# Performance work log

Hardware: AMD Instinct MI355X
Metric: run time of the kernel (lower is better)

## Reference

```python
import jax, jax.numpy as jnp
import numpy as np

BN_EPS = 1e-5


def conv1x1(x, w, b):
    # x: [B,C,H,W], w: [O,C], b: [O]
    return jnp.einsum('oc,bchw->bohw', w, x) + b[None, :, None, None]


def setup_inputs() -> dict:
    key = jax.random.key(0)
    ks = jax.random.split(key, 8)
    B, C, H, W = 4, 256, 64, 64
    Ci = C // 2  # inter_channels
    std = 0.01
    return {
        'x': jax.random.normal(ks[0], (B, C, H, W), dtype=jnp.float32),
        'w_g': jax.random.normal(ks[1], (Ci, C), dtype=jnp.float32) * std,
        'b_g': jnp.zeros((Ci,), jnp.float32),
        'w_theta': jax.random.normal(ks[2], (Ci, C), dtype=jnp.float32) * std,
        'b_theta': jnp.zeros((Ci,), jnp.float32),
        'w_phi': jax.random.normal(ks[3], (Ci, C), dtype=jnp.float32) * std,
        'b_phi': jnp.zeros((Ci,), jnp.float32),
        'w_out': jax.random.normal(ks[4], (C, Ci), dtype=jnp.float32) * std,
        'b_out': jnp.zeros((C,), jnp.float32),
        'bn_gamma': jax.random.normal(ks[5], (C,), dtype=jnp.float32),
        'bn_beta': jnp.zeros((C,), jnp.float32),
    }


def reference(x, w_g, b_g, w_theta, b_theta, w_phi, b_phi, w_out, b_out, bn_gamma, bn_beta):
    B, C, H, W = x.shape
    Ci = w_g.shape[0]
    N = H * W
    # 1x1 conv projections -> flatten spatial to tokens
    g_x = conv1x1(x, w_g, b_g).reshape(B, Ci, N)          # [B,Ci,N]
    theta_x = conv1x1(x, w_theta, b_theta).reshape(B, Ci, N)
    phi_x = conv1x1(x, w_phi, b_phi).reshape(B, Ci, N)
    # dense non-causal attention over N=HW tokens (no scaling)
    f = jnp.einsum('bcn,bcm->bnm', theta_x, phi_x)        # [B,N,N]
    f_div_C = jax.nn.softmax(f, axis=-1)
    y = jnp.einsum('bnm,bcm->bcn', f_div_C, g_x)          # [B,Ci,N]
    y = y.reshape(B, Ci, H, W)
    # output 1x1 conv + BatchNorm2d (training mode: batch statistics)
    W_y = conv1x1(y, w_out, b_out)                        # [B,C,H,W]
    mean = W_y.mean(axis=(0, 2, 3))
    var = W_y.var(axis=(0, 2, 3))
    W_y = (W_y - mean[None, :, None, None]) * jax.lax.rsqrt(var + BN_EPS)[None, :, None, None]
    W_y = W_y * bn_gamma[None, :, None, None] + bn_beta[None, :, None, None]
    return W_y + x
```

## Files before the change

kernel.cpp:

```cpp
#include <hip/hip_runtime.h>

#define N_TOK 4096
#define C_IN 256
#define CI_ 128

typedef unsigned short u16;
typedef unsigned int   u32;
typedef __attribute__((ext_vector_type(8))) short bf16x8;
typedef __attribute__((ext_vector_type(4))) float f32x4;

__device__ __forceinline__ float lo16f(u32 u){ union{u32 i; float f;} c; c.i = u << 16; return c.f; }
__device__ __forceinline__ float hi16f(u32 u){ union{u32 i; float f;} c; c.i = u & 0xffff0000u; return c.f; }
__device__ __forceinline__ void bf8f(const uint4 u, float* f){
    f[0]=lo16f(u.x); f[1]=hi16f(u.x); f[2]=lo16f(u.y); f[3]=hi16f(u.y);
    f[4]=lo16f(u.z); f[5]=hi16f(u.z); f[6]=lo16f(u.w); f[7]=hi16f(u.w);
}
__device__ __forceinline__ float bf1f(u16 v){ union{u32 i; float f;} c; c.i = ((u32)v)<<16; return c.f; }
__device__ __forceinline__ u16 f2bf(float f){
    union{float f; u32 i;} c; c.f = f;
    u32 i = c.i;
    u32 r = (i + 0x7fffu + ((i >> 16) & 1u)) >> 16;
    return (u16)r;
}
__device__ __forceinline__ u32 packbf(float a, float b){
    return (u32)f2bf(a) | ((u32)f2bf(b) << 16);
}

__device__ __forceinline__ void load8(const void* base, size_t idx, int flag, float* f){
    if (flag) {
        const float* p = (const float*)base + idx;
        *(float4*)&f[0] = *(const float4*)p;
        *(float4*)&f[4] = *(const float4*)(p + 4);
    } else {
        uint4 u = *(const uint4*)((const u16*)base + idx);
        bf8f(u, f);
    }
}
__device__ __forceinline__ void load4(const void* base, size_t idx, int flag, float* f){
    if (flag) {
        float4 v = *(const float4*)((const float*)base + idx);
        f[0]=v.x; f[1]=v.y; f[2]=v.z; f[3]=v.w;
    } else {
        uint2 u = *(const uint2*)((const u16*)base + idx);
        f[0]=lo16f(u.x); f[1]=hi16f(u.x); f[2]=lo16f(u.y); f[3]=hi16f(u.y);
    }
}

__device__ __forceinline__ void dma16(const u16* g, char* l){
    __builtin_amdgcn_global_load_lds(
        (const __attribute__((address_space(1))) u32*)g,
        (__attribute__((address_space(3))) u32*)l, 16, 0, 0);
}

__global__ __launch_bounds__(256) void convert_params_kernel(
    const void* wg, const void* wt, const void* wp, const void* wo,
    const void* bg, const void* bt, const void* bp, const void* bo,
    const void* gm, const void* bt2,
    int* __restrict__ flagp, float* __restrict__ canon, u16* __restrict__ canon_bf,
    float* __restrict__ stats)
{
    __shared__ int sflag;
    const int tid = threadIdx.x;
    if (tid < 64) {
        int cnt = 0;
        const u16* wgp = (const u16*)wg;
        for (int i = tid; i < 256; i += 64) {
            u16 v = wgp[2 * i];
            if (((v >> 7) & 0xFF) >= 128) cnt++;
        }
        #pragma unroll
        for (int off = 32; off; off >>= 1) cnt += __shfl_down(cnt, off);
        if (tid == 0) sflag = (cnt >= 8) ? 1 : 0;
    }
    __syncthreads();
    const int f = sflag;
    if (blockIdx.x == 0 && tid == 0) *flagp = f;

    int idx = blockIdx.x * 256 + tid;
    if (idx >= 132224) {
        int j = idx - 132224;
        if (j < 4096) stats[j] = 0.f;
        return;
    }
    const void* src; int loc;
    if      (idx < 32768)  { src = wg;  loc = idx; }
    else if (idx < 65536)  { src = wt;  loc = idx - 32768; }
    else if (idx < 98304)  { src = wp;  loc = idx - 65536; }
    else if (idx < 131072) { src = wo;  loc = idx - 98304; }
    else if (idx < 131200) { src = bg;  loc = idx - 131072; }
    else if (idx < 131328) { src = bt;  loc = idx - 131200; }
    else if (idx < 131456) { src = bp;  loc = idx - 131328; }
    else if (idx < 131712) { src = bo;  loc = idx - 131456; }
    else if (idx < 131968) { src = gm;  loc = idx - 131712; }
    else                   { src = bt2; loc = idx - 131968; }
    float v = f ? ((const float*)src)[loc] : bf1f(((const u16*)src)[loc]);
    canon[idx] = v;
    if (idx < 131072) canon_bf[idx] = f2bf(v);
}

__global__ __launch_bounds__(256) void xpose_kernel(
    const void* __restrict__ x, const int* __restrict__ flagp, u16* __restrict__ xbfT)
{
    __shared__ u16 t[64][72];
    const int flag = *flagp;
    const int b = blockIdx.z, k0 = blockIdx.y * 64, n0 = blockIdx.x * 64;
    const int tid = threadIdx.x;
    const size_t xb = (size_t)b * C_IN * N_TOK;
    {
        int kk = tid >> 4, n4 = (tid & 15) * 4;
        #pragma unroll
        for (int i = 0; i < 4; ++i) {
            float f[4];
            load4(x, xb + (size_t)(k0 + kk + i * 16) * N_TOK + n0 + n4, flag, f);
            #pragma unroll
            for (int j = 0; j < 4; ++j) t[n4 + j][kk + i * 16] = f2bf(f[j]);
        }
    }
    __syncthreads();
    {
        int kq = tid & 3, n = tid >> 2;
        u16* dst = &xbfT[((size_t)b * N_TOK + n0 + n) * C_IN + k0 + kq * 16];
        *(uint4*)(dst + 0) = *(const uint4*)&t[n][kq * 16];
        *(uint4*)(dst + 8) = *(const uint4*)&t[n][kq * 16 + 8];
    }
}

__global__ __launch_bounds__(512) void proj_kernel(
    const u16* __restrict__ xbfT, const float* __restrict__ canon,
    const u16* __restrict__ wbf,
    u16* __restrict__ gbuf, u16* __restrict__ tbufT, u16* __restrict__ pbufT)
{
    __shared__ __align__(16) u16 plds[64 * 400];
    const int b  = blockIdx.y;
    const int n0 = blockIdx.x * 64;
    const int tid = threadIdx.x;
    const int w    = tid >> 6;
    const int lane = tid & 63;
    const int col  = lane & 15;
    const int quad = lane >> 4;
    const int rw   = w * 48;
    const size_t bN = (size_t)b * N_TOK;

    f32x4 acc[3][4];
    #pragma unroll
    for (int i = 0; i < 3; ++i)
        #pragma unroll
        for (int j = 0; j < 4; ++j) acc[i][j] = (f32x4){0.f,0.f,0.f,0.f};

    #pragma unroll
    for (int kc = 0; kc < 8; ++kc) {
        bf16x8 bfr[4];
        #pragma unroll
        for (int nf = 0; nf < 4; ++nf)
            bfr[nf] = *(const bf16x8*)&xbfT[(bN + n0 + nf * 16 + col) * C_IN + kc * 32 + quad * 8];
        #pragma unroll
        for (int rs = 0; rs < 3; ++rs) {
            bf16x8 afr = *(const bf16x8*)&wbf[(size_t)(rw + rs * 16 + col) * 256 + kc * 32 + quad * 8];
            #pragma unroll
            for (int nf = 0; nf < 4; ++nf)
                acc[rs][nf] = __builtin_amdgcn_mfma_f32_16x16x32_bf16(afr, bfr[nf], acc[rs][nf], 0, 0, 0);
        }
    }

    #pragma unroll
    for (int rs = 0; rs < 3; ++rs) {
        int r0 = rw + rs * 16 + quad * 4;
        float b0 = canon[131072 + r0 + 0];
        float b1 = canon[131072 + r0 + 1];
        float b2 = canon[131072 + r0 + 2];
        float b3 = canon[131072 + r0 + 3];
        #pragma unroll
        for (int nf = 0; nf < 4; ++nf) {
            int n = nf * 16 + col;
            uint2 pv;
            pv.x = packbf(acc[rs][nf][0] + b0, acc[rs][nf][1] + b1);
            pv.y = packbf(acc[rs][nf][2] + b2, acc[rs][nf][3] + b3);
            *(uint2*)&plds[n * 400 + r0] = pv;
        }
    }
    __syncthreads();

    {
        int r = tid & 127, nq = tid >> 7;
        u16 tmp[16];
        #pragma unroll
        for (int j = 0; j < 16; ++j) tmp[j] = plds[(nq * 16 + j) * 400 + r];
        u16* dst = &gbuf[((size_t)b * CI_ + r) * N_TOK + n0 + nq * 16];
        *(uint4*)(dst + 0) = *(uint4*)&tmp[0];
        *(uint4*)(dst + 8) = *(uint4*)&tmp[8];
    }
    {
        int n = tid & 63, part = tid >> 6;
        const u16* src = (part < 4) ? &plds[n * 400 + 128 + part * 32]
                                    : &plds[n * 400 + 256 + (part - 4) * 32];
        u16* dst = (part < 4) ? &tbufT[(bN + n0 + n) * CI_ + part * 32]
                              : &pbufT[(bN + n0 + n) * CI_ + (part - 4) * 32];
        #pragma unroll
        for (int v = 0; v < 4; ++v) *(uint4*)(dst + v * 8) = *(const uint4*)(src + v * 8);
    }
}

#define PB2   131072
#define MST2  147456
#define LST2  147712
#define SMEM2 147968

__global__ __launch_bounds__(512) void attn_kernel(
    const u16* __restrict__ tbufT, const u16* __restrict__ pbufT,
    const u16* __restrict__ gbuf,
    const u16* __restrict__ wbf, const float* __restrict__ canon,
    u16* __restrict__ wyb, float* __restrict__ stats)
{
    __shared__ __align__(16) char smem[SMEM2];
    const int b   = blockIdx.y;
    const int q0  = blockIdx.x * 64;
    const int tid = threadIdx.x;
    const int w    = tid >> 6;
    const int lane = tid & 63;
    const int col  = lane & 15;
    const int quad = lane >> 4;
    const int wq   = w & 3;
    const int ms   = w >> 2;
    const int qw   = wq * 16;
    const size_t bN = (size_t)b * N_TOK;
    const size_t bC = (size_t)b * CI_;

    bf16x8 thf[4];
    {
        const u16* tb = tbufT + (bN + q0 + qw + col) * CI_;
        #pragma unroll
        for (int kc = 0; kc < 4; ++kc)
            thf[kc] = *(const bf16x8*)(tb + kc * 32 + quad * 8);
    }

    const u16* sb[8];
    int ldso[8];
    int sstep;
    if (w < 4) {
        int r = lane >> 4, cp = lane & 15;
        sstep = 128 * CI_;
        #pragma unroll
        for (int j = 0; j < 8; ++j) {
            int seg = w * 8 + j, p = seg >> 4, m0 = (seg & 15) * 4;
            int m = m0 + r, h = cp ^ (m & 15);
            sb[j] = pbufT + (bN + p * 64 + m) * CI_ + h * 8;
            ldso[j] = p * 16384 + m0 * 256;
        }
    } else {
        int r = lane >> 3, cp = lane & 7;
        sstep = 128;
        #pragma unroll
        for (int j = 0; j < 8; ++j) {
            int seg = (w - 4) * 8 + j, p = seg >> 4, c0 = (seg & 15) * 8;
            int c = c0 + r, h = cp ^ (c & 7);
            sb[j] = gbuf + (bC + c) * N_TOK + p * 64 + h * 8;
            ldso[j] = 65536 + p * 16384 + c0 * 128;
        }
    }

    f32x4 yacc[8];
    #pragma unroll
    for (int i = 0; i < 8; ++i) yacc[i] = (f32x4){0.f, 0.f, 0.f, 0.f};
    float m_st = -3.0e38f, l_st = 0.f;

    #pragma unroll
    for (int j = 0; j < 8; ++j) dma16(sb[j], smem + ldso[j]);

    for (int s = 0; s < 32; ++s) {
        const int bb = (s & 1) << 15;
        __asm volatile("s_waitcnt lgkmcnt(0)" ::: "memory");
        __asm volatile("s_barrier" ::: "memory");
        if (s < 31) {
            const int nb = ((s + 1) & 1) << 15;
            const size_t so = (size_t)(s + 1) * sstep;
            #pragma unroll
            for (int j = 0; j < 8; ++j) dma16(sb[j] + so, smem + nb + ldso[j]);
            __asm volatile("s_waitcnt vmcnt(8)" ::: "memory");
        } else {
            __asm volatile("s_waitcnt vmcnt(0)" ::: "memory");
        }
        __asm volatile("s_barrier" ::: "memory");

        f32x4 sacc[4];
        #pragma unroll
        for (int i = 0; i < 4; ++i) sacc[i] = (f32x4){0.f, 0.f, 0.f, 0.f};
        #pragma unroll
        for (int kc = 0; kc < 4; ++kc) {
            #pragma unroll
            for (int msub = 0; msub < 4; ++msub) {
                int m = msub * 16 + col;
                int h = kc * 4 + quad;
                bf16x8 af = *(const bf16x8*)(smem + bb + ms * 16384 + m * 256 + ((h ^ (m & 15)) << 4));
                sacc[msub] = __builtin_amdgcn_mfma_f32_16x16x32_bf16(af, thf[kc], sacc[msub], 0, 0, 0);
            }
        }

        float tmax = sacc[0][0];
        #pragma unroll
        for (int i = 0; i < 4; ++i)
            #pragma unroll
            for (int r = 0; r < 4; ++r) tmax = fmaxf(tmax, sacc[i][r]);
        tmax = fmaxf(tmax, __shfl_xor(tmax, 16));
        tmax = fmaxf(tmax, __shfl_xor(tmax, 32));
        float m_new = fmaxf(m_st, tmax);
        float p16[16], ps = 0.f;
        #pragma unroll
        for (int i = 0; i < 4; ++i)
            #pragma unroll
            for (int r = 0; r < 4; ++r) {
                float pv = __expf(sacc[i][r] - m_new);
                p16[i * 4 + r] = pv;
                ps += pv;
            }
        ps += __shfl_xor(ps, 16);
        ps += __shfl_xor(ps, 32);
        float alpha = __expf(m_st - m_new);
        l_st = l_st * alpha + ps;
        m_st = m_new;
        #pragma unroll
        for (int i = 0; i < 8; ++i) {
            yacc[i][0] *= alpha; yacc[i][1] *= alpha;
            yacc[i][2] *= alpha; yacc[i][3] *= alpha;
        }

        {
            char* pb = smem + PB2 + w * 2048 + col * 128;
            #pragma unroll
            for (int msub = 0; msub < 4; ++msub) {
                #pragma unroll
                for (int pr = 0; pr < 2; ++pr) {
                    u32 d = packbf(p16[msub * 4 + pr * 2], p16[msub * 4 + pr * 2 + 1]);
                    int h = msub * 2 + (quad >> 1);
                    *(u32*)(pb + ((h ^ (col & 7)) << 4) + (quad & 1) * 8 + pr * 4) = d;
                }
            }
        }
        __asm volatile("s_waitcnt lgkmcnt(0)" ::: "memory");

        bf16x8 pf[2];
        #pragma unroll
        for (int km = 0; km < 2; ++km) {
            int h = km * 4 + quad;
            pf[km] = *(const bf16x8*)(smem + PB2 + w * 2048 + col * 128 + ((h ^ (col & 7)) << 4));
        }
        #pragma unroll
        for (int csub = 0; csub < 8; ++csub) {
            #pragma unroll
            for (int km = 0; km < 2; ++km) {
                int c = csub * 16 + col;
                int h = km * 4 + quad;
                bf16x8 gf = *(const bf16x8*)(smem + 65536 + bb + ms * 16384 + c * 128 + ((h ^ (c & 7)) << 4));
                yacc[csub] = __builtin_amdgcn_mfma_f32_16x16x32_bf16(gf, pf[km], yacc[csub], 0, 0, 0);
            }
        }
    }

    __syncthreads();
    if (ms == 1) {
        char* mb = smem + wq * 8192 + col * 512;
        #pragma unroll
        for (int csub = 0; csub < 8; ++csub)
            *(f32x4*)(mb + (((csub * 4 + quad) ^ col) << 4)) = yacc[csub];
        if (quad == 0) {
            *(float*)(smem + MST2 + (wq * 16 + col) * 4) = m_st;
            *(float*)(smem + LST2 + (wq * 16 + col) * 4) = l_st;
        }
    }
    __syncthreads();
    if (ms == 0) {
        float m1 = *(const float*)(smem + MST2 + (wq * 16 + col) * 4);
        float l1 = *(const float*)(smem + LST2 + (wq * 16 + col) * 4);
        float M  = fmaxf(m_st, m1);
        float a0 = __expf(m_st - M), a1 = __expf(m1 - M);
        float li = 1.f / (l_st * a0 + l1 * a1);
        float s0 = a0 * li, s1 = a1 * li;
        const char* mb = smem + wq * 8192 + col * 512;
        const int q = qw + col;
        #pragma unroll
        for (int csub = 0; csub < 8; ++csub) {
            f32x4 y1 = *(const f32x4*)(mb + (((csub * 4 + quad) ^ col) << 4));
            uint2 pv;
            pv.x = packbf(yacc[csub][0] * s0 + y1[0] * s1, yacc[csub][1] * s0 + y1[1] * s1);
            pv.y = packbf(yacc[csub][2] * s0 + y1[2] * s1, yacc[csub][3] * s0 + y1[3] * s1);
            int chunk = csub * 2 + (quad >> 1);
            *(uint2*)(smem + 32768 + q * 256 + ((chunk ^ (q & 15)) << 4) + (quad & 1) * 8) = pv;
        }
    }
    __syncthreads();

    const u16* wo = wbf + 98304;
    f32x4 oacc[2][4];
    #pragma unroll
    for (int i = 0; i < 2; ++i)
        #pragma unroll
        for (int j = 0; j < 4; ++j) oacc[i][j] = (f32x4){0.f,0.f,0.f,0.f};
    #pragma unroll
    for (int kc = 0; kc < 4; ++kc) {
        bf16x8 bqf[4];
        #pragma unroll
        for (int qf = 0; qf < 4; ++qf) {
            int q = qf * 16 + col;
            int h = kc * 4 + quad;
            bqf[qf] = *(const bf16x8*)(smem + 32768 + q * 256 + ((h ^ (q & 15)) << 4));
        }
        #pragma unroll
        for (int os = 0; os < 2; ++os) {
            bf16x8 afr = *(const bf16x8*)&wo[(size_t)(w * 32 + os * 16 + col) * CI_ + kc * 32 + quad * 8];
            #pragma unroll
            for (int qf = 0; qf < 4; ++qf)
                oacc[os][qf] = __builtin_amdgcn_mfma_f32_16x16x32_bf16(afr, bqf[qf], oacc[os][qf], 0, 0, 0);
        }
    }
    const int bucket = (blockIdx.x + blockIdx.y) & 7;
    float* sbk = stats + bucket * 512;
    #pragma unroll
    for (int os = 0; os < 2; ++os) {
        int ob = w * 32 + os * 16 + quad * 4;
        #pragma unroll
        for (int i = 0; i < 4; ++i) {
            float bb2 = canon[131456 + ob + i];
            float s1 = 0.f, s2 = 0.f;
            u16* dst = &wyb[((size_t)b * C_IN + ob + i) * N_TOK + q0 + col];
            #pragma unroll
            for (int qf = 0; qf < 4; ++qf) {
                float v = oacc[os][qf][i] + bb2;
                dst[qf * 16] = f2bf(v);
                s1 += v;
                s2 += v * v;
            }
            #pragma unroll
            for (int off = 8; off; off >>= 1) {
                s1 += __shfl_xor(s1, off);
                s2 += __shfl_xor(s2, off);
            }
            if (col == 0) {
                atomicAdd(&sbk[ob + i], s1);
                atomicAdd(&sbk[256 + ob + i], s2);
            }
        }
    }
}

__global__ __launch_bounds__(256) void bnorm_kernel(
    const u16* __restrict__ wyb, const void* __restrict__ x,
    const float* __restrict__ stats,
    const float* __restrict__ canon, const int* __restrict__ flagp,
    void* __restrict__ outv)
{
    const int flag = *flagp;
    size_t base = ((size_t)blockIdx.x * 256 + threadIdx.x) * 8;
    int o = (int)((base >> 12) & 255);
    float sum1 = 0.f, sum2 = 0.f;
    #pragma unroll
    for (int k = 0; k < 8; ++k) {
        sum1 += stats[k * 512 + o];
        sum2 += stats[k * 512 + 256 + o];
    }
    float mean = sum1 * (1.f / 16384.f);
    float var  = sum2 * (1.f / 16384.f) - mean * mean;
    float r = rsqrtf(var + 1e-5f);
    float gm = canon[131712 + o], bt = canon[131968 + o];
    uint4 wu = *(const uint4*)&wyb[base];
    float wv[8]; bf8f(wu, wv);
    float xf[8]; load8(x, base, flag, xf);
    float ov[8];
    #pragma unroll
    for (int i = 0; i < 8; ++i)
        ov[i] = (wv[i] - mean) * r * gm + bt + xf[i];
    if (flag) {
        float* op = (float*)outv + base;
        *(float4*)op       = *(float4*)&ov[0];
        *(float4*)(op + 4) = *(float4*)&ov[4];
    } else {
        uint4 res;
        res.x = packbf(ov[0], ov[1]);
        res.y = packbf(ov[2], ov[3]);
        res.z = packbf(ov[4], ov[5]);
        res.w = packbf(ov[6], ov[7]);
        *(uint4*)((u16*)outv + base) = res;
    }
}

extern "C" void kernel_launch(void* const* d_in, const int* in_sizes, int n_in,
                              void* d_out, int out_size, void* d_ws, size_t ws_size,
                              hipStream_t stream)
{
    const void* x   = d_in[0];
    const void* w_g = d_in[1];
    const void* b_g = d_in[2];
    const void* w_t = d_in[3];
    const void* b_t = d_in[4];
    const void* w_p = d_in[5];
    const void* b_p = d_in[6];
    const void* w_o = d_in[7];
    const void* b_o = d_in[8];
    const void* gm  = d_in[9];
    const void* bt  = d_in[10];

    char* base = (char*)d_ws;
    float* canon    = (float*)base;
    u16*   canon_bf = (u16*)(base + 528896);
    int*   flagp    = (int*)(base + 791040);
    float* stats    = (float*)(base + 791296);
    u16*   gbuf     = (u16*)(base + 1048576);
    u16*   tbufT    = (u16*)(base + 5242880);
    u16*   pbufT    = (u16*)(base + 9437184);
    u16*   wyb      = (u16*)(base + 13631488);
    u16*   xbfT     = (u16*)(base + 22020096);

    convert_params_kernel<<<533, 256, 0, stream>>>(w_g, w_t, w_p, w_o, b_g, b_t, b_p, b_o,
                                                   gm, bt, flagp, canon, canon_bf, stats);
    xpose_kernel<<<dim3(64, 4, 4), 256, 0, stream>>>(x, flagp, xbfT);
    proj_kernel<<<dim3(64, 4), 512, 0, stream>>>(xbfT, canon, canon_bf, gbuf, tbufT, pbufT);
    attn_kernel<<<dim3(64, 4), 512, 0, stream>>>(tbufT, pbufT, gbuf, canon_bf, canon, wyb, stats);
    bnorm_kernel<<<2048, 256, 0, stream>>>(wyb, x, stats, canon, flagp, d_out);
}
```

Before: 188.0 us.

## Fuse param conversion with transpose, and proj/attn/bnorm into one cooperative kernel

Merges the parameter-conversion and x-transpose kernels into a single prep launch, and fuses projection, attention and batch-norm into one cooperative kernel that uses grid-wide syncs in place of kernel boundaries. The aim is to remove launch overheads and inter-kernel gaps across the five-launch pipeline. In exchange it relies on all 256 blocks of 512 threads with about 148KB of shared memory each being co-resident. It also swaps kernel boundaries for grid barriers, and the bnorm phase now runs on only 256 blocks.

```diff
diff --git a/kernel.cpp b/kernel.cpp
--- a/kernel.cpp
+++ b/kernel.cpp
@@ -1,4 +1,6 @@
 #include <hip/hip_runtime.h>
+#include <hip/hip_cooperative_groups.h>
+namespace cg = cooperative_groups;
 
 #define N_TOK 4096
 #define C_IN 256
@@ -52,14 +54,15 @@
         (__attribute__((address_space(3))) u32*)l, 16, 0, 0);
 }
 
-__global__ __launch_bounds__(256) void convert_params_kernel(
-    const void* wg, const void* wt, const void* wp, const void* wo,
+__global__ __launch_bounds__(256) void prep_kernel(
+    const void* x, const void* wg, const void* wt, const void* wp, const void* wo,
     const void* bg, const void* bt, const void* bp, const void* bo,
     const void* gm, const void* bt2,
     int* __restrict__ flagp, float* __restrict__ canon, u16* __restrict__ canon_bf,
-    float* __restrict__ stats)
+    float* __restrict__ stats, u16* __restrict__ xbfT)
 {
     __shared__ int sflag;
+    __shared__ u16 t[64][72];
     const int tid = threadIdx.x;
     if (tid < 64) {
         int cnt = 0;
@@ -73,411 +76,404 @@
         if (tid == 0) sflag = (cnt >= 8) ? 1 : 0;
     }
     __syncthreads();
-    const int f = sflag;
-    if (blockIdx.x == 0 && tid == 0) *flagp = f;
-
-    int idx = blockIdx.x * 256 + tid;
-    if (idx >= 132224) {
-        int j = idx - 132224;
-        if (j < 4096) stats[j] = 0.f;
-        return;
-    }
-    const void* src; int loc;
-    if      (idx < 32768)  { src = wg;  loc = idx; }
-    else if (idx < 65536)  { src = wt;  loc = idx - 32768; }
-    else if (idx < 98304)  { src = wp;  loc = idx - 65536; }
-    else if (idx < 131072) { src = wo;  loc = idx - 98304; }
-    else if (idx < 131200) { src = bg;  loc = idx - 131072; }
-    else if (idx < 131328) { src = bt;  loc = idx - 131200; }
-    else if (idx < 131456) { src = bp;  loc = idx - 131328; }
-    else if (idx < 131712) { src = bo;  loc = idx - 131456; }
-    else if (idx < 131968) { src = gm;  loc = idx - 131712; }
-    else                   { src = bt2; loc = idx - 131968; }
-    float v = f ? ((const float*)src)[loc] : bf1f(((const u16*)src)[loc]);
-    canon[idx] = v;
-    if (idx < 131072) canon_bf[idx] = f2bf(v);
-}
-
-__global__ __launch_bounds__(256) void xpose_kernel(
-    const void* __restrict__ x, const int* __restrict__ flagp, u16* __restrict__ xbfT)
-{
-    __shared__ u16 t[64][72];
-    const int flag = *flagp;
-    const int b = blockIdx.z, k0 = blockIdx.y * 64, n0 = blockIdx.x * 64;
-    const int tid = threadIdx.x;
-    const size_t xb = (size_t)b * C_IN * N_TOK;
-    {
-        int kk = tid >> 4, n4 = (tid & 15) * 4;
-        #pragma unroll
-        for (int i = 0; i < 4; ++i) {
-            float f[4];
-            load4(x, xb + (size_t)(k0 + kk + i * 16) * N_TOK + n0 + n4, flag, f);
-            #pragma unroll
-            for (int j = 0; j < 4; ++j) t[n4 + j][kk + i * 16] = f2bf(f[j]);
-        }
-    }
-    __syncthreads();
-    {
-        int kq = tid & 3, n = tid >> 2;
-        u16* dst = &xbfT[((size_t)b * N_TOK + n0 + n) * C_IN + k0 + kq * 16];
-        *(uint4*)(dst + 0) = *(const uint4*)&t[n][kq * 16];
-        *(uint4*)(dst + 8) = *(const uint4*)&t[n][kq * 16 + 8];
-    }
-}
-
-__global__ __launch_bounds__(512) void proj_kernel(
+    const int flag = sflag;
+    const int bid = blockIdx.x;
+
+    if (bid < 549) {
+        if (bid == 0 && tid == 0) *flagp = flag;
+        int idx = bid * 256 + tid;
+        if (idx >= 132224) {
+            int j = idx - 132224;
+            if (j < 4096) stats[j] = 0.f;
+            return;
+        }
+        const void* src; int loc;
+        if      (idx < 32768)  { src = wg;  loc = idx; }
+        else if (idx < 65536)  { src = wt;  loc = idx - 32768; }
+        else if (idx < 98304)  { src = wp;  loc = idx - 65536; }
+        else if (idx < 131072) { src = wo;  loc = idx - 98304; }
+        else if (idx < 131200) { src = bg;  loc = idx - 131072; }
+        else if (idx < 131328) { src = bt;  loc = idx - 131200; }
+        else if (idx < 131456) { src = bp;  loc = idx - 131328; }
+        else if (idx < 131712) { src = bo;  loc = idx - 131456; }
+        else if (idx < 131968) { src = gm;  loc = idx - 131712; }
+        else                   { src = bt2; loc = idx - 131968; }
+        float v = flag ? ((const float*)src)[loc] : bf1f(((const u16*)src)[loc]);
+        canon[idx] = v;
+        if (idx < 131072) canon_bf[idx] = f2bf(v);
+    } else {
+        int tb = bid - 549;
+        int nb = tb & 63, kb = (tb >> 6) & 3, b = tb >> 8;
+        const int k0 = kb * 64, n0 = nb * 64;
+        const size_t xb = (size_t)b * C_IN * N_TOK;
+        {
+            int kk = tid >> 4, n4 = (tid & 15) * 4;
+            #pragma unroll
+            for (int i = 0; i < 4; ++i) {
+                float f[4];
+                load4(x, xb + (size_t)(k0 + kk + i * 16) * N_TOK + n0 + n4, flag, f);
+                #pragma unroll
+                for (int j = 0; j < 4; ++j) t[n4 + j][kk + i * 16] = f2bf(f[j]);
+            }
+        }
+        __syncthreads();
+        {
+            int kq = tid & 3, n = tid >> 2;
+            u16* dst = &xbfT[((size_t)b * N_TOK + n0 + n) * C_IN + k0 + kq * 16];
+            *(uint4*)(dst + 0) = *(const uint4*)&t[n][kq * 16];
+            *(uint4*)(dst + 8) = *(const uint4*)&t[n][kq * 16 + 8];
+        }
+    }
+}
+
+#define PB2   131072
+#define MST2  147456
+#define LST2  147712
+#define SMEM2 147968
+
+__global__ __launch_bounds__(512) void mega_kernel(
     const u16* __restrict__ xbfT, const float* __restrict__ canon,
     const u16* __restrict__ wbf,
-    u16* __restrict__ gbuf, u16* __restrict__ tbufT, u16* __restrict__ pbufT)
+    u16* __restrict__ gbuf, u16* __restrict__ tbufT, u16* __restrict__ pbufT,
+    u16* __restrict__ wyb, float* __restrict__ stats,
+    const void* __restrict__ x, const int* __restrict__ flagp,
+    void* __restrict__ outv)
 {
-    __shared__ __align__(16) u16 plds[64 * 400];
-    const int b  = blockIdx.y;
-    const int n0 = blockIdx.x * 64;
+    __shared__ __align__(16) char smem[SMEM2];
+    cg::grid_group grid = cg::this_grid();
+    const int bx  = blockIdx.x;
+    const int b   = blockIdx.y;
     const int tid = threadIdx.x;
     const int w    = tid >> 6;
     const int lane = tid & 63;
     const int col  = lane & 15;
     const int quad = lane >> 4;
-    const int rw   = w * 48;
-    const size_t bN = (size_t)b * N_TOK;
-
-    f32x4 acc[3][4];
-    #pragma unroll
-    for (int i = 0; i < 3; ++i)
-        #pragma unroll
-        for (int j = 0; j < 4; ++j) acc[i][j] = (f32x4){0.f,0.f,0.f,0.f};
-
-    #pragma unroll
-    for (int kc = 0; kc < 8; ++kc) {
-        bf16x8 bfr[4];
-        #pragma unroll
-        for (int nf = 0; nf < 4; ++nf)
-            bfr[nf] = *(const bf16x8*)&xbfT[(bN + n0 + nf * 16 + col) * C_IN + kc * 32 + quad * 8];
-        #pragma unroll
-        for (int rs = 0; rs < 3; ++rs) {
-            bf16x8 afr = *(const bf16x8*)&wbf[(size_t)(rw + rs * 16 + col) * 256 + kc * 32 + quad * 8];
-            #pragma unroll
-            for (int nf = 0; nf < 4; ++nf)
-                acc[rs][nf] = __builtin_amdgcn_mfma_f32_16x16x32_bf16(afr, bfr[nf], acc[rs][nf], 0, 0, 0);
-        }
-    }
-
-    #pragma unroll
-    for (int rs = 0; rs < 3; ++rs) {
-        int r0 = rw + rs * 16 + quad * 4;
-        float b0 = canon[131072 + r0 + 0];
-        float b1 = canon[131072 + r0 + 1];
-        float b2 = canon[131072 + r0 + 2];
-        float b3 = canon[131072 + r0 + 3];
-        #pragma unroll
-        for (int nf = 0; nf < 4; ++nf) {
-            int n = nf * 16 + col;
-            uint2 pv;
-            pv.x = packbf(acc[rs][nf][0] + b0, acc[rs][nf][1] + b1);
-            pv.y = packbf(acc[rs][nf][2] + b2, acc[rs][nf][3] + b3);
-            *(uint2*)&plds[n * 400 + r0] = pv;
-        }
-    }
-    __syncthreads();
-
-    {
-        int r = tid & 127, nq = tid >> 7;
-        u16 tmp[16];
-        #pragma unroll
-        for (int j = 0; j < 16; ++j) tmp[j] = plds[(nq * 16 + j) * 400 + r];
-        u16* dst = &gbuf[((size_t)b * CI_ + r) * N_TOK + n0 + nq * 16];
-        *(uint4*)(dst + 0) = *(uint4*)&tmp[0];
-        *(uint4*)(dst + 8) = *(uint4*)&tmp[8];
-    }
-    {
-        int n = tid & 63, part = tid >> 6;
-        const u16* src = (part < 4) ? &plds[n * 400 + 128 + part * 32]
-                                    : &plds[n * 400 + 256 + (part - 4) * 32];
-        u16* dst = (part < 4) ? &tbufT[(bN + n0 + n) * CI_ + part * 32]
-                              : &pbufT[(bN + n0 + n) * CI_ + (part - 4) * 32];
-        #pragma unroll
-        for (int v = 0; v < 4; ++v) *(uint4*)(dst + v * 8) = *(const uint4*)(src + v * 8);
-    }
-}
-
-#define PB2   131072
-#define MST2  147456
-#define LST2  147712
-#define SMEM2 147968
-
-__global__ __launch_bounds__(512) void attn_kernel(
-    const u16* __restrict__ tbufT, const u16* __restrict__ pbufT,
-    const u16* __restrict__ gbuf,
-    const u16* __restrict__ wbf, const float* __restrict__ canon,
-    u16* __restrict__ wyb, float* __restrict__ stats)
-{
-    __shared__ __align__(16) char smem[SMEM2];
-    const int b   = blockIdx.y;
-    const int q0  = blockIdx.x * 64;
-    const int tid = threadIdx.x;
-    const int w    = tid >> 6;
-    const int lane = tid & 63;
-    const int col  = lane & 15;
-    const int quad = lane >> 4;
-    const int wq   = w & 3;
-    const int ms   = w >> 2;
-    const int qw   = wq * 16;
     const size_t bN = (size_t)b * N_TOK;
     const size_t bC = (size_t)b * CI_;
 
-    bf16x8 thf[4];
     {
-        const u16* tb = tbufT + (bN + q0 + qw + col) * CI_;
-        #pragma unroll
-        for (int kc = 0; kc < 4; ++kc)
-            thf[kc] = *(const bf16x8*)(tb + kc * 32 + quad * 8);
-    }
-
-    const u16* sb[8];
-    int ldso[8];
-    int sstep;
-    if (w < 4) {
-        int r = lane >> 4, cp = lane & 15;
-        sstep = 128 * CI_;
-        #pragma unroll
-        for (int j = 0; j < 8; ++j) {
-            int seg = w * 8 + j, p = seg >> 4, m0 = (seg & 15) * 4;
-            int m = m0 + r, h = cp ^ (m & 15);
-            sb[j] = pbufT + (bN + p * 64 + m) * CI_ + h * 8;
-            ldso[j] = p * 16384 + m0 * 256;
-        }
-    } else {
-        int r = lane >> 3, cp = lane & 7;
-        sstep = 128;
-        #pragma unroll
-        for (int j = 0; j < 8; ++j) {
-            int seg = (w - 4) * 8 + j, p = seg >> 4, c0 = (seg & 15) * 8;
-            int c = c0 + r, h = cp ^ (c & 7);
-            sb[j] = gbuf + (bC + c) * N_TOK + p * 64 + h * 8;
-            ldso[j] = 65536 + p * 16384 + c0 * 128;
-        }
-    }
-
-    f32x4 yacc[8];
-    #pragma unroll
-    for (int i = 0; i < 8; ++i) yacc[i] = (f32x4){0.f, 0.f, 0.f, 0.f};
-    float m_st = -3.0e38f, l_st = 0.f;
-
-    #pragma unroll
-    for (int j = 0; j < 8; ++j) dma16(sb[j], smem + ldso[j]);
-
-    for (int s = 0; s < 32; ++s) {
-        const int bb = (s & 1) << 15;
-        __asm volatile("s_waitcnt lgkmcnt(0)" ::: "memory");
-        __asm volatile("s_barrier" ::: "memory");
-        if (s < 31) {
-            const int nb = ((s + 1) & 1) << 15;
-            const size_t so = (size_t)(s + 1) * sstep;
-            #pragma unroll
-            for (int j = 0; j < 8; ++j) dma16(sb[j] + so, smem + nb + ldso[j]);
-            __asm volatile("s_waitcnt vmcnt(8)" ::: "memory");
+        u16* plds = (u16*)smem;
+        const int n0 = bx * 64;
+        const int rw = w * 48;
+        f32x4 acc[3][4];
+        #pragma unroll
+        for (int i = 0; i < 3; ++i)
+            #pragma unroll
+            for (int j = 0; j < 4; ++j) acc[i][j] = (f32x4){0.f,0.f,0.f,0.f};
+
+        #pragma unroll
+        for (int kc = 0; kc < 8; ++kc) {
+            bf16x8 bfr[4];
+            #pragma unroll
+            for (int nf = 0; nf < 4; ++nf)
+                bfr[nf] = *(const bf16x8*)&xbfT[(bN + n0 + nf * 16 + col) * C_IN + kc * 32 + quad * 8];
+            #pragma unroll
+            for (int rs = 0; rs < 3; ++rs) {
+                bf16x8 afr = *(const bf16x8*)&wbf[(size_t)(rw + rs * 16 + col) * 256 + kc * 32 + quad * 8];
+                #pragma unroll
+                for (int nf = 0; nf < 4; ++nf)
+                    acc[rs][nf] = __builtin_amdgcn_mfma_f32_16x16x32_bf16(afr, bfr[nf], acc[rs][nf], 0, 0, 0);
+            }
+        }
+        #pragma unroll
+        for (int rs = 0; rs < 3; ++rs) {
+            int r0 = rw + rs * 16 + quad * 4;
+            float b0 = canon[131072 + r0 + 0];
+            float b1 = canon[131072 + r0 + 1];
+            float b2 = canon[131072 + r0 + 2];
+            float b3 = canon[131072 + r0 + 3];
+            #pragma unroll
+            for (int nf = 0; nf < 4; ++nf) {
+                int n = nf * 16 + col;
+                uint2 pv;
+                pv.x = packbf(acc[rs][nf][0] + b0, acc[rs][nf][1] + b1);
+                pv.y = packbf(acc[rs][nf][2] + b2, acc[rs][nf][3] + b3);
+                *(uint2*)&plds[n * 400 + r0] = pv;
+            }
+        }
+        __syncthreads();
+        {
+            int r = tid & 127, nq = tid >> 7;
+            u16 tmp[16];
+            #pragma unroll
+            for (int j = 0; j < 16; ++j) tmp[j] = plds[(nq * 16 + j) * 400 + r];
+            u16* dst = &gbuf[(bC + r) * N_TOK + n0 + nq * 16];
+            *(uint4*)(dst + 0) = *(uint4*)&tmp[0];
+            *(uint4*)(dst + 8) = *(uint4*)&tmp[8];
+        }
+        {
+            int n = tid & 63, part = tid >> 6;
+            const u16* src = (part < 4) ? &plds[n * 400 + 128 + part * 32]
+                                        : &plds[n * 400 + 256 + (part - 4) * 32];
+            u16* dst = (part < 4) ? &tbufT[(bN + n0 + n) * CI_ + part * 32]
+                                  : &pbufT[(bN + n0 + n) * CI_ + (part - 4) * 32];
+            #pragma unroll
+            for (int v = 0; v < 4; ++v) *(uint4*)(dst + v * 8) = *(const uint4*)(src + v * 8);
+        }
+    }
+    grid.sync();
+
+    {
+        const int q0 = bx * 64;
+        const int wq = w & 3;
+        const int ms = w >> 2;
+        const int qw = wq * 16;
+
+        bf16x8 thf[4];
+        {
+            const u16* tb = tbufT + (bN + q0 + qw + col) * CI_;
+            #pragma unroll
+            for (int kc = 0; kc < 4; ++kc)
+                thf[kc] = *(const bf16x8*)(tb + kc * 32 + quad * 8);
+        }
+
+        const u16* sbp[8];
+        int ldso[8];
+        int sstep;
+        if (w < 4) {
+            int r = lane >> 4, cp = lane & 15;
+            sstep = 128 * CI_;
+            #pragma unroll
+            for (int j = 0; j < 8; ++j) {
+                int seg = w * 8 + j, p = seg >> 4, m0 = (seg & 15) * 4;
+                int m = m0 + r, h = cp ^ (m & 15);
+                sbp[j] = pbufT + (bN + p * 64 + m) * CI_ + h * 8;
+                ldso[j] = p * 16384 + m0 * 256;
+            }
         } else {
-            __asm volatile("s_waitcnt vmcnt(0)" ::: "memory");
-        }
-        __asm volatile("s_barrier" ::: "memory");
-
-        f32x4 sacc[4];
-        #pragma unroll
-        for (int i = 0; i < 4; ++i) sacc[i] = (f32x4){0.f, 0.f, 0.f, 0.f};
+            int r = lane >> 3, cp = lane & 7;
+            sstep = 128;
+            #pragma unroll
+            for (int j = 0; j < 8; ++j) {
+                int seg = (w - 4) * 8 + j, p = seg >> 4, c0 = (seg & 15) * 8;
+                int c = c0 + r, h = cp ^ (c & 7);
+                sbp[j] = gbuf + (bC + c) * N_TOK + p * 64 + h * 8;
+                ldso[j] = 65536 + p * 16384 + c0 * 128;
+            }
+        }
+
+        f32x4 yacc[8];
+        #pragma unroll
+        for (int i = 0; i < 8; ++i) yacc[i] = (f32x4){0.f, 0.f, 0.f, 0.f};
+        float m_st = -3.0e38f, l_st = 0.f;
+
+        #pragma unroll
+        for (int j = 0; j < 8; ++j) dma16(sbp[j], smem + ldso[j]);
+
+        for (int s = 0; s < 32; ++s) {
+            const int bb = (s & 1) << 15;
+            __asm volatile("s_waitcnt lgkmcnt(0)" ::: "memory");
+            __asm volatile("s_barrier" ::: "memory");
+            if (s < 31) {
+                const int nb = ((s + 1) & 1) << 15;
+                const size_t so = (size_t)(s + 1) * sstep;
+                #pragma unroll
+                for (int j = 0; j < 8; ++j) dma16(sbp[j] + so, smem + nb + ldso[j]);
+                __asm volatile("s_waitcnt vmcnt(8)" ::: "memory");
+            } else {
+                __asm volatile("s_waitcnt vmcnt(0)" ::: "memory");
+            }
+            __asm volatile("s_barrier" ::: "memory");
+
+            f32x4 sacc[4];
+            #pragma unroll
+            for (int i = 0; i < 4; ++i) sacc[i] = (f32x4){0.f, 0.f, 0.f, 0.f};
+            #pragma unroll
+            for (int kc = 0; kc < 4; ++kc) {
+                #pragma unroll
+                for (int msub = 0; msub < 4; ++msub) {
+                    int m = msub * 16 + col;
+                    int h = kc * 4 + quad;
+                    bf16x8 af = *(const bf16x8*)(smem + bb + ms * 16384 + m * 256 + ((h ^ (m & 15)) << 4));
+                    sacc[msub] = __builtin_amdgcn_mfma_f32_16x16x32_bf16(af, thf[kc], sacc[msub], 0, 0, 0);
+                }
+            }
+
+            float tmax = sacc[0][0];
+            #pragma unroll
+            for (int i = 0; i < 4; ++i)
+                #pragma unroll
+                for (int r = 0; r < 4; ++r) tmax = fmaxf(tmax, sacc[i][r]);
+            tmax = fmaxf(tmax, __shfl_xor(tmax, 16));
+            tmax = fmaxf(tmax, __shfl_xor(tmax, 32));
+            float m_new = fmaxf(m_st, tmax);
+            float p16[16], ps = 0.f;
+            #pragma unroll
+            for (int i = 0; i < 4; ++i)
+                #pragma unroll
+                for (int r = 0; r < 4; ++r) {
+                    float pv = __expf(sacc[i][r] - m_new);
+                    p16[i * 4 + r] = pv;
+                    ps += pv;
+                }
+            ps += __shfl_xor(ps, 16);
+            ps += __shfl_xor(ps, 32);
+            float alpha = __expf(m_st - m_new);
+            l_st = l_st * alpha + ps;
+            m_st = m_new;
+            #pragma unroll
+            for (int i = 0; i < 8; ++i) {
+                yacc[i][0] *= alpha; yacc[i][1] *= alpha;
+                yacc[i][2] *= alpha; yacc[i][3] *= alpha;
+            }
+
+            {
+                char* pb = smem + PB2 + w * 2048 + col * 128;
+                #pragma unroll
+                for (int msub = 0; msub < 4; ++msub) {
+                    #pragma unroll
+                    for (int pr = 0; pr < 2; ++pr) {
+                        u32 d = packbf(p16[msub * 4 + pr * 2], p16[msub * 4 + pr * 2 + 1]);
+                        int h = msub * 2 + (quad >> 1);
+                        *(u32*)(pb + ((h ^ (col & 7)) << 4) + (quad & 1) * 8 + pr * 4) = d;
+                    }
+                }
+            }
+            __asm volatile("s_waitcnt lgkmcnt(0)" ::: "memory");
+
+            bf16x8 pf[2];
+            #pragma unroll
+            for (int km = 0; km < 2; ++km) {
+                int h = km * 4 + quad;
+                pf[km] = *(const bf16x8*)(smem + PB2 + w * 2048 + col * 128 + ((h ^ (col & 7)) << 4));
+            }
+            #pragma unroll
+            for (int csub = 0; csub < 8; ++csub) {
+                #pragma unroll
+                for (int km = 0; km < 2; ++km) {
+                    int c = csub * 16 + col;
+                    int h = km * 4 + quad;
+                    bf16x8 gf = *(const bf16x8*)(smem + 65536 + bb + ms * 16384 + c * 128 + ((h ^ (c & 7)) << 4));
+                    yacc[csub] = __builtin_amdgcn_mfma_f32_16x16x32_bf16(gf, pf[km], yacc[csub], 0, 0, 0);
+                }
+            }
+        }
+
+        __syncthreads();
+        if (ms == 1) {
+            char* mb = smem + wq * 8192 + col * 512;
+            #pragma unroll
+            for (int csub = 0; csub < 8; ++csub)
+                *(f32x4*)(mb + (((csub * 4 + quad) ^ col) << 4)) = yacc[csub];
+            if (quad == 0) {
+                *(float*)(smem + MST2 + (wq * 16 + col) * 4) = m_st;
+                *(float*)(smem + LST2 + (wq * 16 + col) * 4) = l_st;
+            }
+        }
+        __syncthreads();
+        if (ms == 0) {
+            float m1 = *(const float*)(smem + MST2 + (wq * 16 + col) * 4);
+            float l1 = *(const float*)(smem + LST2 + (wq * 16 + col) * 4);
+            float M  = fmaxf(m_st, m1);
+            float a0 = __expf(m_st - M), a1 = __expf(m1 - M);
+            float li = 1.f / (l_st * a0 + l1 * a1);
+            float s0 = a0 * li, s1 = a1 * li;
+            const char* mb = smem + wq * 8192 + col * 512;
+            const int q = qw + col;
+            #pragma unroll
+            for (int csub = 0; csub < 8; ++csub) {
+                f32x4 y1 = *(const f32x4*)(mb + (((csub * 4 + quad) ^ col) << 4));
+                uint2 pv;
+                pv.x = packbf(yacc[csub][0] * s0 + y1[0] * s1, yacc[csub][1] * s0 + y1[1] * s1);
+                pv.y = packbf(yacc[csub][2] * s0 + y1[2] * s1, yacc[csub][3] * s0 + y1[3] * s1);
+                int chunk = csub * 2 + (quad >> 1);
+                *(uint2*)(smem + 32768 + q * 256 + ((chunk ^ (q & 15)) << 4) + (quad & 1) * 8) = pv;
+            }
+        }
+        __syncthreads();
+
+        const u16* wo = wbf + 98304;
+        f32x4 oacc[2][4];
+        #pragma unroll
+        for (int i = 0; i < 2; ++i)
+            #pragma unroll
+            for (int j = 0; j < 4; ++j) oacc[i][j] = (f32x4){0.f,0.f,0.f,0.f};
         #pragma unroll
         for (int kc = 0; kc < 4; ++kc) {
-            #pragma unroll
-            for (int msub = 0; msub < 4; ++msub) {
-                int m = msub * 16 + col;
+            bf16x8 bqf[4];
+            #pragma unroll
+            for (int qf = 0; qf < 4; ++qf) {
+                int q = qf * 16 + col;
                 int h = kc * 4 + quad;
-                bf16x8 af = *(const bf16x8*)(smem + bb + ms * 16384 + m * 256 + ((h ^ (m & 15)) << 4));
-                sacc[msub] = __builtin_amdgcn_mfma_f32_16x16x32_bf16(af, thf[kc], sacc[msub], 0, 0, 0);
-            }
-        }
-
-        float tmax = sacc[0][0];
-        #pragma unroll
-        for (int i = 0; i < 4; ++i)
-            #pragma unroll
-            for (int r = 0; r < 4; ++r) tmax = fmaxf(tmax, sacc[i][r]);
-        tmax = fmaxf(tmax, __shfl_xor(tmax, 16));
-        tmax = fmaxf(tmax, __shfl_xor(tmax, 32));
-        float m_new = fmaxf(m_st, tmax);
-        float p16[16], ps = 0.f;
-        #pragma unroll
-        for (int i = 0; i < 4; ++i)
-            #pragma unroll
-            for (int r = 0; r < 4; ++r) {
-                float pv = __expf(sacc[i][r] - m_new);
-                p16[i * 4 + r] = pv;
-                ps += pv;
-            }
-        ps += __shfl_xor(ps, 16);
-        ps += __shfl_xor(ps, 32);
-        float alpha = __expf(m_st - m_new);
-        l_st = l_st * alpha + ps;
-        m_st = m_new;
-        #pragma unroll
-        for (int i = 0; i < 8; ++i) {
-            yacc[i][0] *= alpha; yacc[i][1] *= alpha;
-            yacc[i][2] *= alpha; yacc[i][3] *= alpha;
-        }
-
-        {
-            char* pb = smem + PB2 + w * 2048 + col * 128;
-            #pragma unroll
-            for (int msub = 0; msub < 4; ++msub) {
-                #pragma unroll
-                for (int pr = 0; pr < 2; ++pr) {
-                    u32 d = packbf(p16[msub * 4 + pr * 2], p16[msub * 4 + pr * 2 + 1]);
-                    int h = msub * 2 + (quad >> 1);
-                    *(u32*)(pb + ((h ^ (col & 7)) << 4) + (quad & 1) * 8 + pr * 4) = d;
-                }
-            }
-        }
-        __asm volatile("s_waitcnt lgkmcnt(0)" ::: "memory");
-
-        bf16x8 pf[2];
-        #pragma unroll
-        for (int km = 0; km < 2; ++km) {
-            int h = km * 4 + quad;
-            pf[km] = *(const bf16x8*)(smem + PB2 + w * 2048 + col * 128 + ((h ^ (col & 7)) << 4));
-        }
-        #pragma unroll
-        for (int csub = 0; csub < 8; ++csub) {
-            #pragma unroll
-            for (int km = 0; km < 2; ++km) {
-                int c = csub * 16 + col;
-                int h = km * 4 + quad;
-                bf16x8 gf = *(const bf16x8*)(smem + 65536 + bb + ms * 16384 + c * 128 + ((h ^ (c & 7)) << 4));
-                yacc[csub] = __builtin_amdgcn_mfma_f32_16x16x32_bf16(gf, pf[km], yacc[csub], 0, 0, 0);
-            }
-        }
-    }
-
-    __syncthreads();
-    if (ms == 1) {
-        char* mb = smem + wq * 8192 + col * 512;
-        #pragma unroll
-        for (int csub = 0; csub < 8; ++csub)
-            *(f32x4*)(mb + (((csub * 4 + quad) ^ col) << 4)) = yacc[csub];
-        if (quad == 0) {
-            *(float*)(smem + MST2 + (wq * 16 + col) * 4) = m_st;
-            *(float*)(smem + LST2 + (wq * 16 + col) * 4) = l_st;
-        }
-    }
-    __syncthreads();
-    if (ms == 0) {
-        float m1 = *(const float*)(smem + MST2 + (wq * 16 + col) * 4);
-        float l1 = *(const float*)(smem + LST2 + (wq * 16 + col) * 4);
-        float M  = fmaxf(m_st, m1);
-        float a0 = __expf(m_st - M), a1 = __expf(m1 - M);
-        float li = 1.f / (l_st * a0 + l1 * a1);
-        float s0 = a0 * li, s1 = a1 * li;
-        const char* mb = smem + wq * 8192 + col * 512;
-        const int q = qw + col;
-        #pragma unroll
-        for (int csub = 0; csub < 8; ++csub) {
-            f32x4 y1 = *(const f32x4*)(mb + (((csub * 4 + quad) ^ col) << 4));
-            uint2 pv;
-            pv.x = packbf(yacc[csub][0] * s0 + y1[0] * s1, yacc[csub][1] * s0 + y1[1] * s1);
-            pv.y = packbf(yacc[csub][2] * s0 + y1[2] * s1, yacc[csub][3] * s0 + y1[3] * s1);
-            int chunk = csub * 2 + (quad >> 1);
-            *(uint2*)(smem + 32768 + q * 256 + ((chunk ^ (q & 15)) << 4) + (quad & 1) * 8) = pv;
-        }
-    }
-    __syncthreads();
-
-    const u16* wo = wbf + 98304;
-    f32x4 oacc[2][4];
-    #pragma unroll
-    for (int i = 0; i < 2; ++i)
-        #pragma unroll
-        for (int j = 0; j < 4; ++j) oacc[i][j] = (f32x4){0.f,0.f,0.f,0.f};
-    #pragma unroll
-    for (int kc = 0; kc < 4; ++kc) {
-        bf16x8 bqf[4];
-        #pragma unroll
-        for (int qf = 0; qf < 4; ++qf) {
-            int q = qf * 16 + col;
-            int h = kc * 4 + quad;
-            bqf[qf] = *(const bf16x8*)(smem + 32768 + q * 256 + ((h ^ (q & 15)) << 4));
-        }
+                bqf[qf] = *(const bf16x8*)(smem + 32768 + q * 256 + ((h ^ (q & 15)) << 4));
+            }
+            #pragma unroll
+            for (int os = 0; os < 2; ++os) {
+                bf16x8 afr = *(const bf16x8*)&wo[(size_t)(w * 32 + os * 16 + col) * CI_ + kc * 32 + quad * 8];
+                #pragma unroll
+                for (int qf = 0; qf < 4; ++qf)
+                    oacc[os][qf] = __builtin_amdgcn_mfma_f32_16x16x32_bf16(afr, bqf[qf], oacc[os][qf], 0, 0, 0);
+            }
+        }
+        const int bucket = (bx + b) & 7;
+        float* sbk = stats + bucket * 512;
         #pragma unroll
         for (int os = 0; os < 2; ++os) {
-            bf16x8 afr = *(const bf16x8*)&wo[(size_t)(w * 32 + os * 16 + col) * CI_ + kc * 32 + quad * 8];
-            #pragma unroll
-            for (int qf = 0; qf < 4; ++qf)
-                oacc[os][qf] = __builtin_amdgcn_mfma_f32_16x16x32_bf16(afr, bqf[qf], oacc[os][qf], 0, 0, 0);
-        }
-    }
-    const int bucket = (blockIdx.x + blockIdx.y) & 7;
-    float* sbk = stats + bucket * 512;
-    #pragma unroll
-    for (int os = 0; os < 2; ++os) {
-        int ob = w * 32 + os * 16 + quad * 4;
-        #pragma unroll
-        for (int i = 0; i < 4; ++i) {
-            float bb2 = canon[131456 + ob + i];
-            float s1 = 0.f, s2 = 0.f;
-            u16* dst = &wyb[((size_t)b * C_IN + ob + i) * N_TOK + q0 + col];
-            #pragma unroll
-            for (int qf = 0; qf < 4; ++qf) {
-                float v = oacc[os][qf][i] + bb2;
-                dst[qf * 16] = f2bf(v);
-                s1 += v;
-                s2 += v * v;
-            }
-            #pragma unroll
-            for (int off = 8; off; off >>= 1) {
-                s1 += __shfl_xor(s1, off);
-                s2 += __shfl_xor(s2, off);
-            }
-            if (col == 0) {
-                atomicAdd(&sbk[ob + i], s1);
-                atomicAdd(&sbk[256 + ob + i], s2);
-            }
-        }
-    }
-}
-
-__global__ __launch_bounds__(256) void bnorm_kernel(
-    const u16* __restrict__ wyb, const void* __restrict__ x,
-    const float* __restrict__ stats,
-    const float* __restrict__ canon, const int* __restrict__ flagp,
-    void* __restrict__ outv)
-{
-    const int flag = *flagp;
-    size_t base = ((size_t)blockIdx.x * 256 + threadIdx.x) * 8;
-    int o = (int)((base >> 12) & 255);
-    float sum1 = 0.f, sum2 = 0.f;
-    #pragma unroll
-    for (int k = 0; k < 8; ++k) {
-        sum1 += stats[k * 512 + o];
-        sum2 += stats[k * 512 + 256 + o];
-    }
-    float mean = sum1 * (1.f / 16384.f);
-    float var  = sum2 * (1.f / 16384.f) - mean * mean;
-    float r = rsqrtf(var + 1e-5f);
-    float gm = canon[131712 + o], bt = canon[131968 + o];
-    uint4 wu = *(const uint4*)&wyb[base];
-    float wv[8]; bf8f(wu, wv);
-    float xf[8]; load8(x, base, flag, xf);
-    float ov[8];
-    #pragma unroll
-    for (int i = 0; i < 8; ++i)
-        ov[i] = (wv[i] - mean) * r * gm + bt + xf[i];
-    if (flag) {
-        float* op = (float*)outv + base;
-        *(float4*)op       = *(float4*)&ov[0];
-        *(float4*)(op + 4) = *(float4*)&ov[4];
-    } else {
-        uint4 res;
-        res.x = packbf(ov[0], ov[1]);
-        res.y = packbf(ov[2], ov[3]);
-        res.z = packbf(ov[4], ov[5]);
-        res.w = packbf(ov[6], ov[7]);
-        *(uint4*)((u16*)outv + base) = res;
+            int ob = w * 32 + os * 16 + quad * 4;
+            #pragma unroll
+            for (int i = 0; i < 4; ++i) {
+                float bb2 = canon[131456 + ob + i];
+                float s1 = 0.f, s2 = 0.f;
+                u16* dst = &wyb[((size_t)b * C_IN + ob + i) * N_TOK + q0 + col];
+                #pragma unroll
+                for (int qf = 0; qf < 4; ++qf) {
+                    float v = oacc[os][qf][i] + bb2;
+                    dst[qf * 16] = f2bf(v);
+                    s1 += v;
+                    s2 += v * v;
+                }
+                #pragma unroll
+                for (int off = 8; off; off >>= 1) {
+                    s1 += __shfl_xor(s1, off);
+                    s2 += __shfl_xor(s2, off);
+                }
+                if (col == 0) {
+                    atomicAdd(&sbk[ob + i], s1);
+                    atomicAdd(&sbk[256 + ob + i], s2);
+                }
+            }
+        }
+    }
+    grid.sync();
+
+    {
+        const int flag = *flagp;
+        const int o = bx * 4 + (tid >> 7);
+        const int l128 = tid & 127;
+        float sum1 = 0.f, sum2 = 0.f;
+        #pragma unroll
+        for (int k = 0; k < 8; ++k) {
+            sum1 += stats[k * 512 + o];
+            sum2 += stats[k * 512 + 256 + o];
+        }
+        float mean = sum1 * (1.f / 16384.f);
+        float var  = sum2 * (1.f / 16384.f) - mean * mean;
+        float r = rsqrtf(var + 1e-5f);
+        float gmv = canon[131712 + o], btv = canon[131968 + o];
+        const size_t rowb = ((size_t)b * C_IN + o) * N_TOK;
+        #pragma unroll
+        for (int j = 0; j < 4; ++j) {
+            size_t base = rowb + (size_t)l128 * 32 + j * 8;
+            uint4 wu = *(const uint4*)&wyb[base];
+            float wv[8]; bf8f(wu, wv);
+            float xf[8]; load8(x, base, flag, xf);
+            float ov[8];
+            #pragma unroll
+            for (int i = 0; i < 8; ++i)
+                ov[i] = (wv[i] - mean) * r * gmv + btv + xf[i];
+            if (flag) {
+                float* op = (float*)outv + base;
+                *(float4*)op       = *(float4*)&ov[0];
+                *(float4*)(op + 4) = *(float4*)&ov[4];
+            } else {
+                uint4 res;
+                res.x = packbf(ov[0], ov[1]);
+                res.y = packbf(ov[2], ov[3]);
+                res.z = packbf(ov[4], ov[5]);
+                res.w = packbf(ov[6], ov[7]);
+                *(uint4*)((u16*)outv + base) = res;
+            }
+        }
     }
 }
 
@@ -508,10 +504,13 @@
     u16*   wyb      = (u16*)(base + 13631488);
     u16*   xbfT     = (u16*)(base + 22020096);
 
-    convert_params_kernel<<<533, 256, 0, stream>>>(w_g, w_t, w_p, w_o, b_g, b_t, b_p, b_o,
-                                                   gm, bt, flagp, canon, canon_bf, stats);
-    xpose_kernel<<<dim3(64, 4, 4), 256, 0, stream>>>(x, flagp, xbfT);
-    proj_kernel<<<dim3(64, 4), 512, 0, stream>>>(xbfT, canon, canon_bf, gbuf, tbufT, pbufT);
-    attn_kernel<<<dim3(64, 4), 512, 0, stream>>>(tbufT, pbufT, gbuf, canon_bf, canon, wyb, stats);
-    bnorm_kernel<<<2048, 256, 0, stream>>>(wyb, x, stats, canon, flagp, d_out);
-}
+    prep_kernel<<<1573, 256, 0, stream>>>(x, w_g, w_t, w_p, w_o, b_g, b_t, b_p, b_o,
+                                          gm, bt, flagp, canon, canon_bf, stats, xbfT);
+
+    void* outp = d_out;
+    void* args[] = {(void*)&xbfT, (void*)&canon, (void*)&canon_bf,
+                    (void*)&gbuf, (void*)&tbufT, (void*)&pbufT,
+                    (void*)&wyb, (void*)&stats, (void*)&x, (void*)&flagp, (void*)&outp};
+    hipLaunchCooperativeKernel((void*)mega_kernel, dim3(64, 4), dim3(512, 1, 1),
+                               args, 0, stream);
+}
```

Measured after the change: 286.3 us. 52.3% more time.
